# Kernel optimization log

Measured on AMD Instinct MI355X. Metric: run time of the kernel, lower is better.

## Reference

```python
import jax, jax.numpy as jnp
import numpy as np

B, N, K, C = 4, 8192, 16, 128
T = 3  # num_iterations


def _gather(x, idx):
    # x: (B, N, C), idx: (B, N, K) -> (B, N, K, C)
    return jax.vmap(lambda a, i: a[i])(x, idx)


def _linear(x, W, b):
    # torch nn.Linear convention: W is (out, in)
    return x @ W.T + b


def setup_inputs() -> dict:
    key = jax.random.key(0)
    ks = jax.random.split(key, 20)
    s = 0.05
    inp = {
        'xyz': jax.random.normal(ks[0], (B, N, 3), jnp.float32),
        'features': jax.random.normal(ks[1], (B, N, C), jnp.float32),
        'knn_idx': jax.random.randint(ks[2], (B, N, K), 0, N),
        # offset_pred: Linear(C,C) -> ReLU -> Linear(C,3)
        'off_W1': jax.random.normal(ks[3], (C, C), jnp.float32) * s,
        'off_b1': jnp.zeros((C,), jnp.float32),
        'off_W2': jax.random.normal(ks[4], (3, C), jnp.float32) * s,
        'off_b2': jnp.zeros((3,), jnp.float32),
        # per-iteration edge MLP: Linear(3+C, C) -> ReLU -> Linear(C, C)
        'edge_W1': jax.random.normal(ks[5], (T, C, 3 + C), jnp.float32) * s,
        'edge_b1': jnp.zeros((T, C), jnp.float32),
        'edge_W2': jax.random.normal(ks[6], (T, C, C), jnp.float32) * s,
        'edge_b2': jnp.zeros((T, C), jnp.float32),
        # per-iteration update MLP: Linear(2C, C) -> ReLU -> Linear(C, C)
        'upd_W1': jax.random.normal(ks[7], (T, C, 2 * C), jnp.float32) * s,
        'upd_b1': jnp.zeros((T, C), jnp.float32),
        'upd_W2': jax.random.normal(ks[8], (T, C, C), jnp.float32) * s,
        'upd_b2': jnp.zeros((T, C), jnp.float32),
    }
    return inp


def reference(xyz, features, knn_idx, off_W1, off_b1, off_W2, off_b2,
              edge_W1, edge_b1, edge_W2, edge_b2,
              upd_W1, upd_b1, upd_W2, upd_b2):
    n_iter = edge_W1.shape[0]
    for t in range(n_iter):
        delta_xyz = _linear(jax.nn.relu(_linear(features, off_W1, off_b1)), off_W2, off_b2)
        neighbor_xyz = _gather(xyz, knn_idx)          # (B,N,K,3)
        neighbor_feat = _gather(features, knn_idx)    # (B,N,K,C)
        center_xyz = xyz + delta_xyz                  # (B,N,3)
        rel_pos = neighbor_xyz - center_xyz[:, :, None, :]
        edge_input = jnp.concatenate([rel_pos, neighbor_feat], axis=-1)  # (B,N,K,3+C)
        edge_feat = _linear(jax.nn.relu(_linear(edge_input, edge_W1[t], edge_b1[t])), edge_W2[t], edge_b2[t])
        agg_feat = jnp.max(edge_feat, axis=2)         # (B,N,C)
        upd_in = jnp.concatenate([agg_feat, features], axis=-1)
        features = features + _linear(jax.nn.relu(_linear(upd_in, upd_W1[t], upd_b1[t])), upd_W2[t], upd_b2[t])
    return features
```

## Files before the change

kernel.cpp:

```cpp
#include <hip/hip_runtime.h>
#include <cstddef>

#define NB 4
#define NP 8192
#define NK 16
#define NC 128
#define HW_ 136
#define GIW 136
#define AGW 136
#define CW  132
#define UINW 264
#define HUW 136

using short8   = __attribute__((ext_vector_type(8))) short;
using ushort4v = __attribute__((ext_vector_type(4))) unsigned short;
using floatx4  = __attribute__((ext_vector_type(4))) float;

union U8 { short8 s8; unsigned u[4]; };

__device__ __forceinline__ unsigned short f2bf(float f) {
    union { float f; unsigned u; } v; v.f = f;
    unsigned r = v.u + 0x7FFFu + ((v.u >> 16) & 1u);
    return (unsigned short)(r >> 16);
}
__device__ __forceinline__ float bf2f(unsigned short u) {
    union { unsigned u; float f; } v; v.u = ((unsigned)u) << 16;
    return v.f;
}
__device__ __forceinline__ unsigned cvt_pk_bf16(float lo, float hi) {
    unsigned d;
    asm("v_cvt_pk_bf16_f32 %0, %1, %2" : "=v"(d) : "v"(lo), "v"(hi));
    return d;
}

#define MFMA(a, b, c) __builtin_amdgcn_mfma_f32_16x16x32_bf16((a), (b), (c), 0, 0, 0)

__device__ __forceinline__ short8 xform(short8 g, floatx4 ca, floatx4 cb) {
    U8 u;
    u.u[0] = cvt_pk_bf16(fmaxf(bf2f((unsigned short)g[0]) - ca[0], 0.f),
                         fmaxf(bf2f((unsigned short)g[1]) - ca[1], 0.f));
    u.u[1] = cvt_pk_bf16(fmaxf(bf2f((unsigned short)g[2]) - ca[2], 0.f),
                         fmaxf(bf2f((unsigned short)g[3]) - ca[3], 0.f));
    u.u[2] = cvt_pk_bf16(fmaxf(bf2f((unsigned short)g[4]) - cb[0], 0.f),
                         fmaxf(bf2f((unsigned short)g[5]) - cb[1], 0.f));
    u.u[3] = cvt_pk_bf16(fmaxf(bf2f((unsigned short)g[6]) - cb[2], 0.f),
                         fmaxf(bf2f((unsigned short)g[7]) - cb[3], 0.f));
    return u.s8;
}

__global__ void pack_weights_k(const float* __restrict__ offW1,
                               const float* __restrict__ eW1,
                               const float* __restrict__ eW2,
                               const float* __restrict__ uW1,
                               const float* __restrict__ uW2,
                               unsigned short* __restrict__ offW1p,
                               unsigned short* __restrict__ eW1fp,
                               unsigned short* __restrict__ eW2p,
                               unsigned short* __restrict__ uW1p,
                               unsigned short* __restrict__ uW2p)
{
    int i = blockIdx.x * 256 + threadIdx.x;
    if (i < 16384) { offW1p[i] = f2bf(offW1[i]); return; }
    i -= 16384;
    if (i < 49152) {
        int tt = i / 16384, rem = i % 16384;
        int o = rem / 128, k = rem % 128;
        eW1fp[i] = f2bf(eW1[(tt * 128 + o) * 131 + 3 + k]);
        return;
    }
    i -= 49152;
    if (i < 49152) { eW2p[i] = f2bf(eW2[i]); return; }
    i -= 49152;
    if (i < 98304) { uW1p[i] = f2bf(uW1[i]); return; }
    i -= 98304;
    if (i < 49152) { uW2p[i] = f2bf(uW2[i]); }
}

__global__ __launch_bounds__(256, 4)
void center_k(const float* __restrict__ Fin, const float* __restrict__ xyz,
              const unsigned short* __restrict__ offW1p,
              const float* __restrict__ offW2, const float* __restrict__ offb1,
              const float* __restrict__ offb2,
              const unsigned short* __restrict__ eW1fp,
              const float* __restrict__ eW1r0,
              const float* __restrict__ eb1_0,
              unsigned short* __restrict__ Gbf, float* __restrict__ ctr)
{
    __shared__ __align__(16) unsigned short sA[32 * HW_];
    __shared__ __align__(16) unsigned short sH[32 * HW_];
    __shared__ float s_XY[96];
    const int t = threadIdx.x, wv = t >> 6, ln = t & 63, q = ln >> 4, r = ln & 15;
    const int cg0 = wv << 1;
    const int base = blockIdx.x * 32;

    {
        int row = t >> 3, c16 = (t & 7) * 16;
        const float* src = Fin + (size_t)(base + row) * NC + c16;
        float4 f0 = *(const float4*)src;
        float4 f1 = *(const float4*)(src + 4);
        float4 f2 = *(const float4*)(src + 8);
        float4 f3 = *(const float4*)(src + 12);
        short8 u0, u1;
        u0[0]=f2bf(f0.x); u0[1]=f2bf(f0.y); u0[2]=f2bf(f0.z); u0[3]=f2bf(f0.w);
        u0[4]=f2bf(f1.x); u0[5]=f2bf(f1.y); u0[6]=f2bf(f1.z); u0[7]=f2bf(f1.w);
        u1[0]=f2bf(f2.x); u1[1]=f2bf(f2.y); u1[2]=f2bf(f2.z); u1[3]=f2bf(f2.w);
        u1[4]=f2bf(f3.x); u1[5]=f2bf(f3.y); u1[6]=f2bf(f3.z); u1[7]=f2bf(f3.w);
        *(short8*)&sA[row * HW_ + c16]     = u0;
        *(short8*)&sA[row * HW_ + c16 + 8] = u1;
    }
    if (t < 96) s_XY[t] = xyz[(size_t)base * 3 + t];
    __syncthreads();

    floatx4 agk[2][2];
    {
        short8 wo[2][4], wg[2][4];
#pragma unroll
        for (int c = 0; c < 2; ++c)
#pragma unroll
            for (int ks = 0; ks < 4; ++ks) {
                wo[c][ks] = *(const short8*)(offW1p + ((cg0 + c) * 16 + r) * NC + ks * 32 + q * 8);
                wg[c][ks] = *(const short8*)(eW1fp  + ((cg0 + c) * 16 + r) * NC + ks * 32 + q * 8);
            }
        float bo[2] = { offb1[cg0 * 16 + r], offb1[(cg0 + 1) * 16 + r] };
#pragma unroll
        for (int rt = 0; rt < 2; ++rt) {
            short8 af[4];
#pragma unroll
            for (int ks = 0; ks < 4; ++ks)
                af[ks] = *(const short8*)&sA[(rt * 16 + r) * HW_ + ks * 32 + q * 8];
            floatx4 ao[2] = { {0.f,0.f,0.f,0.f}, {0.f,0.f,0.f,0.f} };
            floatx4 ag[2] = { {0.f,0.f,0.f,0.f}, {0.f,0.f,0.f,0.f} };
#pragma unroll
            for (int c = 0; c < 2; ++c)
#pragma unroll
                for (int ks = 0; ks < 4; ++ks) {
                    ao[c] = MFMA(af[ks], wo[c][ks], ao[c]);
                    ag[c] = MFMA(af[ks], wg[c][ks], ag[c]);
                }
#pragma unroll
            for (int c = 0; c < 2; ++c) {
                int col = (cg0 + c) * 16 + r;
#pragma unroll
                for (int i = 0; i < 4; ++i)
                    sH[(rt * 16 + q * 4 + i) * HW_ + col] = f2bf(fmaxf(ao[c][i] + bo[c], 0.f));
                agk[rt][c] = ag[c];
            }
        }
    }
    __syncthreads();

    {
#pragma unroll
        for (int c = 0; c < 2; ++c) {
            int col = (cg0 + c) * 16 + r;
            const float* wN = eW1r0 + (size_t)col * 131;
            float w0 = wN[0], w1 = wN[1], w2 = wN[2], b1v = eb1_0[col];
#pragma unroll
            for (int rt = 0; rt < 2; ++rt)
#pragma unroll
                for (int i = 0; i < 4; ++i) {
                    int row = rt * 16 + q * 4 + i;
                    sA[row * HW_ + col] = f2bf(agk[rt][c][i]
                        + s_XY[row * 3 + 0] * w0 + s_XY[row * 3 + 1] * w1
                        + s_XY[row * 3 + 2] * w2 + b1v);
                }
        }
    }
    if (wv < 2) {
        int rt = wv;
        short8 wf[4];
#pragma unroll
        for (int ks = 0; ks < 4; ++ks) {
            short8 u = {0,0,0,0,0,0,0,0};
            if (r < 3) {
                const float* w = offW2 + r * NC + ks * 32 + q * 8;
                float4 f0 = *(const float4*)w;
                float4 f1 = *(const float4*)(w + 4);
                u[0]=f2bf(f0.x); u[1]=f2bf(f0.y); u[2]=f2bf(f0.z); u[3]=f2bf(f0.w);
                u[4]=f2bf(f1.x); u[5]=f2bf(f1.y); u[6]=f2bf(f1.z); u[7]=f2bf(f1.w);
            }
            wf[ks] = u;
        }
        short8 af[4];
#pragma unroll
        for (int ks = 0; ks < 4; ++ks)
            af[ks] = *(const short8*)&sH[(rt * 16 + r) * HW_ + ks * 32 + q * 8];
        floatx4 acc = {0.f, 0.f, 0.f, 0.f};
#pragma unroll
        for (int ks = 0; ks < 4; ++ks)
            acc = MFMA(af[ks], wf[ks], acc);
        if (r < 3) {
#pragma unroll
            for (int i = 0; i < 4; ++i) {
                int p = rt * 16 + q * 4 + i;
                ctr[(size_t)(base + p) * 3 + r] =
                    xyz[(size_t)(base + p) * 3 + r] + acc[i] + offb2[r];
            }
        }
    }
    __syncthreads();

    {
        int row = t >> 3, c16 = (t & 7) * 16;
        *(short8*)(Gbf + (size_t)(base + row) * NC + c16)     = *(short8*)&sA[row * HW_ + c16];
        *(short8*)(Gbf + (size_t)(base + row) * NC + c16 + 8) = *(short8*)&sA[row * HW_ + c16 + 8];
    }
}

__global__ __launch_bounds__(256, 2)
void edge_k(const unsigned short* __restrict__ Gbf,
            const int* __restrict__ knn,
            const float* __restrict__ ctr,
            const float* __restrict__ eW1rC,
            const float* __restrict__ eb2,
            const unsigned short* __restrict__ eW2p,
            unsigned short* __restrict__ aggG)
{
    __shared__ __align__(16) unsigned short s_H[64 * GIW];
    __shared__ __align__(16) float s_C[8 * CW];
    __shared__ __align__(16) unsigned short s_AGB[8 * AGW];

    const int xcd  = blockIdx.x & 7;
    const int slot = blockIdx.x >> 3;
    const int b    = xcd >> 1;
    const int n0   = ((slot << 1) | (xcd & 1)) << 3;
    const int t = threadIdx.x, wv = t >> 6, ln = t & 63;
    const int q = ln >> 4, r = ln & 15, cg0 = wv << 1;
    const int base = b * NP + n0;
    const int rr = t >> 4, c8 = (t & 15) * 8;

    const int* kb = knn + (size_t)base * NK;
    int kn[8];
#pragma unroll
    for (int j = 0; j < 8; ++j) kn[j] = kb[j * 16 + rr];
    short8 g0[4];
#pragma unroll
    for (int p = 0; p < 4; ++p)
        g0[p] = *(const short8*)(Gbf + (size_t)(b * NP + kn[p]) * NC + c8);

    short8 wf2[2][4];
#pragma unroll
    for (int c = 0; c < 2; ++c)
#pragma unroll
        for (int ks = 0; ks < 4; ++ks)
            wf2[c][ks] = *(const short8*)(eW2p + ((cg0 + c) * 16 + r) * NC + ks * 32 + q * 8);
    float eb2v[2] = { eb2[cg0 * 16 + r], eb2[(cg0 + 1) * 16 + r] };

    {
        int p = t >> 5, c0 = (t & 31) * 4;
        float cx = ctr[(size_t)(base + p) * 3 + 0];
        float cy = ctr[(size_t)(base + p) * 3 + 1];
        float cz = ctr[(size_t)(base + p) * 3 + 2];
#pragma unroll
        for (int k = 0; k < 4; ++k) {
            int col = c0 + k;
            const float* w = eW1rC + (size_t)col * 131;
            s_C[p * CW + col] = cx * w[0] + cy * w[1] + cz * w[2];
        }
    }
    __syncthreads();

#pragma unroll
    for (int p = 0; p < 4; ++p) {
        const float* cp = &s_C[p * CW + c8];
        floatx4 ca = *(const floatx4*)(cp);
        floatx4 cb = *(const floatx4*)(cp + 4);
        *(short8*)&s_H[(p * 16 + rr) * GIW + c8] = xform(g0[p], ca, cb);
    }
    short8 g1[4];
#pragma unroll
    for (int p = 0; p < 4; ++p)
        g1[p] = *(const short8*)(Gbf + (size_t)(b * NP + kn[4 + p]) * NC + c8);
    __syncthreads();

#pragma unroll
    for (int rt = 0; rt < 4; ++rt) {
        short8 af[4];
#pragma unroll
        for (int ks = 0; ks < 4; ++ks)
            af[ks] = *(const short8*)&s_H[(rt * 16 + r) * GIW + ks * 32 + q * 8];
        floatx4 acc[2] = { {0.f,0.f,0.f,0.f}, {0.f,0.f,0.f,0.f} };
#pragma unroll
        for (int c = 0; c < 2; ++c)
#pragma unroll
            for (int ks = 0; ks < 4; ++ks)
                acc[c] = MFMA(af[ks], wf2[c][ks], acc[c]);
#pragma unroll
        for (int c = 0; c < 2; ++c) {
            float m = fmaxf(fmaxf(acc[c][0], acc[c][1]), fmaxf(acc[c][2], acc[c][3]));
            m = fmaxf(m, __shfl_xor(m, 16));
            m = fmaxf(m, __shfl_xor(m, 32));
            if (q == 0)
                s_AGB[rt * AGW + (cg0 + c) * 16 + r] = f2bf(m + eb2v[c]);
        }
    }
    __syncthreads();

#pragma unroll
    for (int p = 0; p < 4; ++p) {
        const float* cp = &s_C[(4 + p) * CW + c8];
        floatx4 ca = *(const floatx4*)(cp);
        floatx4 cb = *(const floatx4*)(cp + 4);
        *(short8*)&s_H[(p * 16 + rr) * GIW + c8] = xform(g1[p], ca, cb);
    }
    __syncthreads();

#pragma unroll
    for (int rt = 0; rt < 4; ++rt) {
        short8 af[4];
#pragma unroll
        for (int ks = 0; ks < 4; ++ks)
            af[ks] = *(const short8*)&s_H[(rt * 16 + r) * GIW + ks * 32 + q * 8];
        floatx4 acc[2] = { {0.f,0.f,0.f,0.f}, {0.f,0.f,0.f,0.f} };
#pragma unroll
        for (int c = 0; c < 2; ++c)
#pragma unroll
            for (int ks = 0; ks < 4; ++ks)
                acc[c] = MFMA(af[ks], wf2[c][ks], acc[c]);
#pragma unroll
        for (int c = 0; c < 2; ++c) {
            float m = fmaxf(fmaxf(acc[c][0], acc[c][1]), fmaxf(acc[c][2], acc[c][3]));
            m = fmaxf(m, __shfl_xor(m, 16));
            m = fmaxf(m, __shfl_xor(m, 32));
            if (q == 0)
                s_AGB[(4 + rt) * AGW + (cg0 + c) * 16 + r] = f2bf(m + eb2v[c]);
        }
    }
    __syncthreads();

    if (t < 128) {
        int row = t >> 4, cc = (t & 15) * 8;
        *(short8*)(aggG + (size_t)(base + row) * NC + cc) = *(short8*)&s_AGB[row * AGW + cc];
    }
}

__global__ __launch_bounds__(256, 3)
void upd_k(const float* __restrict__ Fin, float* __restrict__ Fout,
           const unsigned short* __restrict__ aggG,
           const float* __restrict__ xyz,
           const unsigned short* __restrict__ uW1p,
           const unsigned short* __restrict__ uW2p,
           const float* __restrict__ ub1, const float* __restrict__ ub2,
           const unsigned short* __restrict__ eW1fpN,
           const float* __restrict__ eW1rN,
           const float* __restrict__ eb1N,
           const unsigned short* __restrict__ offW1p,
           const float* __restrict__ offW2, const float* __restrict__ offb1,
           const float* __restrict__ offb2,
           unsigned short* __restrict__ Gbf, float* __restrict__ ctrOut,
           int doNext)
{
    __shared__ __align__(16) unsigned short s_UIN[32 * UINW];
    __shared__ __align__(16) unsigned short s_H[32 * HUW];
    __shared__ __align__(16) unsigned short s_FN[32 * HUW];
    __shared__ float s_XY[96];

    const int xcd  = blockIdx.x & 7;
    const int slot = blockIdx.x >> 3;
    const int b    = xcd >> 1;
    const int n0   = ((slot << 1) | (xcd & 1)) << 5;
    const int t = threadIdx.x, wv = t >> 6, ln = t & 63;
    const int q = ln >> 4, r = ln & 15, cg0 = wv << 1;
    const int base = b * NP + n0;
    const int row32 = t >> 3, c16 = (t & 7) * 16;

    {
        const unsigned short* ap = aggG + (size_t)(base + row32) * NC + c16;
        *(short8*)&s_UIN[row32 * UINW + c16]     = *(const short8*)ap;
        *(short8*)&s_UIN[row32 * UINW + c16 + 8] = *(const short8*)(ap + 8);
        const float* src = Fin + (size_t)(base + row32) * NC + c16;
        float4 f0 = *(const float4*)src;
        float4 f1 = *(const float4*)(src + 4);
        float4 f2 = *(const float4*)(src + 8);
        float4 f3 = *(const float4*)(src + 12);
        short8 u0, u1;
        u0[0]=f2bf(f0.x); u0[1]=f2bf(f0.y); u0[2]=f2bf(f0.z); u0[3]=f2bf(f0.w);
        u0[4]=f2bf(f1.x); u0[5]=f2bf(f1.y); u0[6]=f2bf(f1.z); u0[7]=f2bf(f1.w);
        u1[0]=f2bf(f2.x); u1[1]=f2bf(f2.y); u1[2]=f2bf(f2.z); u1[3]=f2bf(f2.w);
        u1[4]=f2bf(f3.x); u1[5]=f2bf(f3.y); u1[6]=f2bf(f3.z); u1[7]=f2bf(f3.w);
        *(short8*)&s_UIN[row32 * UINW + 128 + c16]     = u0;
        *(short8*)&s_UIN[row32 * UINW + 128 + c16 + 8] = u1;
    }
    if (t < 96) s_XY[t] = xyz[(size_t)base * 3 + t];
    __syncthreads();

    {
        short8 wfa[2][8];
#pragma unroll
        for (int c = 0; c < 2; ++c)
#pragma unroll
            for (int ks = 0; ks < 8; ++ks)
                wfa[c][ks] = *(const short8*)(uW1p + ((cg0 + c) * 16 + r) * 256 + ks * 32 + q * 8);
        float ub1v[2] = { ub1[cg0 * 16 + r], ub1[(cg0 + 1) * 16 + r] };
#pragma unroll
        for (int rt = 0; rt < 2; ++rt) {
            short8 af[8];
#pragma unroll
            for (int ks = 0; ks < 8; ++ks)
                af[ks] = *(const short8*)&s_UIN[(rt * 16 + r) * UINW + ks * 32 + q * 8];
            floatx4 acc3[2] = { {0.f,0.f,0.f,0.f}, {0.f,0.f,0.f,0.f} };
#pragma unroll
            for (int c = 0; c < 2; ++c)
#pragma unroll
                for (int ks = 0; ks < 8; ++ks)
                    acc3[c] = MFMA(af[ks], wfa[c][ks], acc3[c]);
#pragma unroll
            for (int c = 0; c < 2; ++c)
#pragma unroll
                for (int i = 0; i < 4; ++i)
                    s_H[(rt * 16 + q * 4 + i) * HUW + (cg0 + c) * 16 + r] =
                        f2bf(fmaxf(acc3[c][i] + ub1v[c], 0.f));
        }
    }
    __syncthreads();

    {
        short8 wfb[2][4];
#pragma unroll
        for (int c = 0; c < 2; ++c)
#pragma unroll
            for (int ks = 0; ks < 4; ++ks)
                wfb[c][ks] = *(const short8*)(uW2p + ((cg0 + c) * 16 + r) * NC + ks * 32 + q * 8);
        float ub2v[2] = { ub2[cg0 * 16 + r], ub2[(cg0 + 1) * 16 + r] };
#pragma unroll
        for (int rt = 0; rt < 2; ++rt) {
            short8 af[4];
#pragma unroll
            for (int ks = 0; ks < 4; ++ks)
                af[ks] = *(const short8*)&s_H[(rt * 16 + r) * HUW + ks * 32 + q * 8];
            floatx4 acc[2] = { {0.f,0.f,0.f,0.f}, {0.f,0.f,0.f,0.f} };
#pragma unroll
            for (int c = 0; c < 2; ++c)
#pragma unroll
                for (int ks = 0; ks < 4; ++ks)
                    acc[c] = MFMA(af[ks], wfb[c][ks], acc[c]);
#pragma unroll
            for (int c = 0; c < 2; ++c) {
                int col = (cg0 + c) * 16 + r;
#pragma unroll
                for (int i = 0; i < 4; ++i) {
                    int p = rt * 16 + q * 4 + i;
                    float fnew = Fin[(size_t)(base + p) * NC + col] + acc[c][i] + ub2v[c];
                    Fout[(size_t)(base + p) * NC + col] = fnew;
                    s_FN[p * HUW + col] = f2bf(fnew);
                }
            }
        }
    }

    if (doNext) {
        __syncthreads();
        {
            short8 wg[2][4], wo[2][4];
#pragma unroll
            for (int c = 0; c < 2; ++c)
#pragma unroll
                for (int ks = 0; ks < 4; ++ks) {
                    wg[c][ks] = *(const short8*)(eW1fpN + ((cg0 + c) * 16 + r) * NC + ks * 32 + q * 8);
                    wo[c][ks] = *(const short8*)(offW1p + ((cg0 + c) * 16 + r) * NC + ks * 32 + q * 8);
                }
            float bo[2] = { offb1[cg0 * 16 + r], offb1[(cg0 + 1) * 16 + r] };
#pragma unroll
            for (int rt = 0; rt < 2; ++rt) {
                short8 af[4];
#pragma unroll
                for (int ks = 0; ks < 4; ++ks)
                    af[ks] = *(const short8*)&s_FN[(rt * 16 + r) * HUW + ks * 32 + q * 8];
                floatx4 ag[2] = { {0.f,0.f,0.f,0.f}, {0.f,0.f,0.f,0.f} };
                floatx4 ao[2] = { {0.f,0.f,0.f,0.f}, {0.f,0.f,0.f,0.f} };
#pragma unroll
                for (int c = 0; c < 2; ++c)
#pragma unroll
                    for (int ks = 0; ks < 4; ++ks) {
                        ag[c] = MFMA(af[ks], wg[c][ks], ag[c]);
                        ao[c] = MFMA(af[ks], wo[c][ks], ao[c]);
                    }
#pragma unroll
                for (int c = 0; c < 2; ++c) {
                    int col = (cg0 + c) * 16 + r;
                    const float* wN = eW1rN + (size_t)col * 131;
                    float w0 = wN[0], w1 = wN[1], w2 = wN[2], b1v = eb1N[col];
#pragma unroll
                    for (int i = 0; i < 4; ++i) {
                        int p = rt * 16 + q * 4 + i;
                        s_UIN[p * UINW + col] = f2bf(ag[c][i]
                            + s_XY[p * 3 + 0] * w0 + s_XY[p * 3 + 1] * w1
                            + s_XY[p * 3 + 2] * w2 + b1v);
                        s_H[p * HUW + col]    = f2bf(fmaxf(ao[c][i] + bo[c], 0.f));
                    }
                }
            }
        }
        __syncthreads();

        *(short8*)(Gbf + (size_t)(base + row32) * NC + c16) =
            *(short8*)&s_UIN[row32 * UINW + c16];
        *(short8*)(Gbf + (size_t)(base + row32) * NC + c16 + 8) =
            *(short8*)&s_UIN[row32 * UINW + c16 + 8];

        if (wv < 2) {
            int rt = wv;
            short8 wf[4];
#pragma unroll
            for (int ks = 0; ks < 4; ++ks) {
                short8 u = {0,0,0,0,0,0,0,0};
                if (r < 3) {
                    const float* w = offW2 + r * NC + ks * 32 + q * 8;
                    float4 f0 = *(const float4*)w;
                    float4 f1 = *(const float4*)(w + 4);
                    u[0]=f2bf(f0.x); u[1]=f2bf(f0.y); u[2]=f2bf(f0.z); u[3]=f2bf(f0.w);
                    u[4]=f2bf(f1.x); u[5]=f2bf(f1.y); u[6]=f2bf(f1.z); u[7]=f2bf(f1.w);
                }
                wf[ks] = u;
            }
            short8 af[4];
#pragma unroll
            for (int ks = 0; ks < 4; ++ks)
                af[ks] = *(const short8*)&s_H[(rt * 16 + r) * HUW + ks * 32 + q * 8];
            floatx4 acc = {0.f, 0.f, 0.f, 0.f};
#pragma unroll
            for (int ks = 0; ks < 4; ++ks)
                acc = MFMA(af[ks], wf[ks], acc);
            if (r < 3) {
#pragma unroll
                for (int i = 0; i < 4; ++i) {
                    int p = rt * 16 + q * 4 + i;
                    ctrOut[(size_t)(base + p) * 3 + r] =
                        xyz[(size_t)(base + p) * 3 + r] + acc[i] + offb2[r];
                }
            }
        }
    }
}

extern "C" void kernel_launch(void* const* d_in, const int* in_sizes, int n_in,
                              void* d_out, int out_size, void* d_ws, size_t ws_size,
                              hipStream_t stream)
{
    const float* xyz   = (const float*)d_in[0];
    const float* feat  = (const float*)d_in[1];
    const int*   knn   = (const int*)d_in[2];
    const float* offW1 = (const float*)d_in[3];
    const float* offb1 = (const float*)d_in[4];
    const float* offW2 = (const float*)d_in[5];
    const float* offb2 = (const float*)d_in[6];
    const float* eW1   = (const float*)d_in[7];
    const float* eb1   = (const float*)d_in[8];
    const float* eW2   = (const float*)d_in[9];
    const float* eb2   = (const float*)d_in[10];
    const float* uW1   = (const float*)d_in[11];
    const float* ub1   = (const float*)d_in[12];
    const float* uW2   = (const float*)d_in[13];
    const float* ub2   = (const float*)d_in[14];
    float* out = (float*)d_out;

    char* ws = (char*)d_ws;
    unsigned short* Gbf    = (unsigned short*)ws;
    float*          ctrb   = (float*)(ws + 8388608);
    unsigned short* offW1p = (unsigned short*)(ws + 8781824);
    unsigned short* eW1fp  = (unsigned short*)(ws + 8814592);
    unsigned short* eW2p   = (unsigned short*)(ws + 8912896);
    unsigned short* uW1p   = (unsigned short*)(ws + 9011200);
    unsigned short* uW2p   = (unsigned short*)(ws + 9207808);
    unsigned short* aggG   = (unsigned short*)(ws + 9306112);

    pack_weights_k<<<1024, 256, 0, stream>>>(offW1, eW1, eW2, uW1, uW2,
                                             offW1p, eW1fp, eW2p, uW1p, uW2p);

    center_k<<<1024, 256, 0, stream>>>(feat, xyz, offW1p, offW2,
                                       offb1, offb2, eW1fp, eW1, eb1,
                                       Gbf, ctrb);

    for (int tt = 0; tt < 3; ++tt) {
        int ntt = (tt + 1) % 3;
        edge_k<<<4096, 256, 0, stream>>>(
            Gbf, knn, ctrb,
            eW1 + (size_t)tt * 128 * 131, eb2 + tt * 128,
            eW2p + tt * 16384, aggG);
        const float* fin = (tt == 0) ? feat : out;
        upd_k<<<1024, 256, 0, stream>>>(
            fin, out, aggG, xyz,
            uW1p + tt * 32768, uW2p + tt * 16384, ub1 + tt * 128, ub2 + tt * 128,
            eW1fp + ntt * 16384, eW1 + (size_t)ntt * 128 * 131, eb1 + ntt * 128,
            offW1p, offW2, offb1, offb2,
            Gbf, ctrb, (tt < 2) ? 1 : 0);
    }
}
```

Before: 295.9 us.

## Restructure edge kernel to gather neighbors directly into MFMA A-fragments per wave

The edge kernel now handles 16 points per block with half as many blocks. Each wave owns four points, gathers neighbor features straight into MFMA A-operand registers, and loops over all 8 output column groups using the W2 weights staged once in shared memory. This removes the s_H shared-memory staging and several block barriers, and amortizes the W2 load over more points. In exchange it uses more LDS per block (the full 128x136 W2 tile) and issues per-lane 16-byte gathers that may coalesce less well.

```diff
diff --git a/kernel.cpp b/kernel.cpp
--- a/kernel.cpp
+++ b/kernel.cpp
@@ -6,7 +6,7 @@
 #define NK 16
 #define NC 128
 #define HW_ 136
-#define GIW 136
+#define SW2 136
 #define AGW 136
 #define CW  132
 #define UINW 264
@@ -216,119 +216,86 @@
             const unsigned short* __restrict__ eW2p,
             unsigned short* __restrict__ aggG)
 {
-    __shared__ __align__(16) unsigned short s_H[64 * GIW];
-    __shared__ __align__(16) float s_C[8 * CW];
-    __shared__ __align__(16) unsigned short s_AGB[8 * AGW];
+    __shared__ __align__(16) unsigned short s_W2[128 * SW2];
+    __shared__ __align__(16) float s_C[16 * CW];
+    __shared__ __align__(16) unsigned short s_AGB[16 * AGW];
 
     const int xcd  = blockIdx.x & 7;
     const int slot = blockIdx.x >> 3;
     const int b    = xcd >> 1;
-    const int n0   = ((slot << 1) | (xcd & 1)) << 3;
+    const int n0   = ((slot << 1) | (xcd & 1)) << 4;
     const int t = threadIdx.x, wv = t >> 6, ln = t & 63;
-    const int q = ln >> 4, r = ln & 15, cg0 = wv << 1;
+    const int q = ln >> 4, r = ln & 15;
     const int base = b * NP + n0;
-    const int rr = t >> 4, c8 = (t & 15) * 8;
-
-    const int* kb = knn + (size_t)base * NK;
-    int kn[8];
-#pragma unroll
-    for (int j = 0; j < 8; ++j) kn[j] = kb[j * 16 + rr];
-    short8 g0[4];
-#pragma unroll
-    for (int p = 0; p < 4; ++p)
-        g0[p] = *(const short8*)(Gbf + (size_t)(b * NP + kn[p]) * NC + c8);
-
-    short8 wf2[2][4];
-#pragma unroll
-    for (int c = 0; c < 2; ++c)
-#pragma unroll
-        for (int ks = 0; ks < 4; ++ks)
-            wf2[c][ks] = *(const short8*)(eW2p + ((cg0 + c) * 16 + r) * NC + ks * 32 + q * 8);
-    float eb2v[2] = { eb2[cg0 * 16 + r], eb2[(cg0 + 1) * 16 + r] };
-
-    {
-        int p = t >> 5, c0 = (t & 31) * 4;
+    const int wp0 = wv << 2;
+
+    {
+        int row = t >> 1, c64 = (t & 1) << 6;
+        const unsigned short* src = eW2p + row * NC + c64;
+#pragma unroll
+        for (int g = 0; g < 8; ++g)
+            *(short8*)&s_W2[row * SW2 + c64 + g * 8] = *(const short8*)(src + g * 8);
+    }
+    {
+        int p = t >> 4, c0 = (t & 15) * 8;
         float cx = ctr[(size_t)(base + p) * 3 + 0];
         float cy = ctr[(size_t)(base + p) * 3 + 1];
         float cz = ctr[(size_t)(base + p) * 3 + 2];
 #pragma unroll
-        for (int k = 0; k < 4; ++k) {
+        for (int k = 0; k < 8; ++k) {
             int col = c0 + k;
             const float* w = eW1rC + (size_t)col * 131;
             s_C[p * CW + col] = cx * w[0] + cy * w[1] + cz * w[2];
         }
     }
-    __syncthreads();
-
-#pragma unroll
-    for (int p = 0; p < 4; ++p) {
-        const float* cp = &s_C[p * CW + c8];
-        floatx4 ca = *(const floatx4*)(cp);
-        floatx4 cb = *(const floatx4*)(cp + 4);
-        *(short8*)&s_H[(p * 16 + rr) * GIW + c8] = xform(g0[p], ca, cb);
-    }
-    short8 g1[4];
+    float ebv[8];
+#pragma unroll
+    for (int c = 0; c < 8; ++c) ebv[c] = eb2[c * 16 + r];
+    int kn[4];
 #pragma unroll
     for (int p = 0; p < 4; ++p)
-        g1[p] = *(const short8*)(Gbf + (size_t)(b * NP + kn[4 + p]) * NC + c8);
-    __syncthreads();
-
-#pragma unroll
-    for (int rt = 0; rt < 4; ++rt) {
-        short8 af[4];
-#pragma unroll
-        for (int ks = 0; ks < 4; ++ks)
-            af[ks] = *(const short8*)&s_H[(rt * 16 + r) * GIW + ks * 32 + q * 8];
-        floatx4 acc[2] = { {0.f,0.f,0.f,0.f}, {0.f,0.f,0.f,0.f} };
-#pragma unroll
-        for (int c = 0; c < 2; ++c)
+        kn[p] = knn[(size_t)(base + wp0 + p) * NK + r];
+    __syncthreads();
+
+#pragma unroll
+    for (int pair = 0; pair < 2; ++pair) {
+        short8 haf[2][4];
+#pragma unroll
+        for (int pp = 0; pp < 2; ++pp) {
+            int p = pair * 2 + pp;
+            const unsigned short* gp = Gbf + (size_t)(b * NP + kn[p]) * NC + q * 8;
+            const float* cp = &s_C[(wp0 + p) * CW + q * 8];
+#pragma unroll
+            for (int ks = 0; ks < 4; ++ks) {
+                short8 g = *(const short8*)(gp + ks * 32);
+                floatx4 ca = *(const floatx4*)(cp + ks * 32);
+                floatx4 cb = *(const floatx4*)(cp + ks * 32 + 4);
+                haf[pp][ks] = xform(g, ca, cb);
+            }
+        }
+#pragma unroll
+        for (int c = 0; c < 8; ++c) {
+            short8 bf[4];
 #pragma unroll
             for (int ks = 0; ks < 4; ++ks)
-                acc[c] = MFMA(af[ks], wf2[c][ks], acc[c]);
-#pragma unroll
-        for (int c = 0; c < 2; ++c) {
-            float m = fmaxf(fmaxf(acc[c][0], acc[c][1]), fmaxf(acc[c][2], acc[c][3]));
-            m = fmaxf(m, __shfl_xor(m, 16));
-            m = fmaxf(m, __shfl_xor(m, 32));
-            if (q == 0)
-                s_AGB[rt * AGW + (cg0 + c) * 16 + r] = f2bf(m + eb2v[c]);
-        }
-    }
-    __syncthreads();
-
-#pragma unroll
-    for (int p = 0; p < 4; ++p) {
-        const float* cp = &s_C[(4 + p) * CW + c8];
-        floatx4 ca = *(const floatx4*)(cp);
-        floatx4 cb = *(const floatx4*)(cp + 4);
-        *(short8*)&s_H[(p * 16 + rr) * GIW + c8] = xform(g1[p], ca, cb);
-    }
-    __syncthreads();
-
-#pragma unroll
-    for (int rt = 0; rt < 4; ++rt) {
-        short8 af[4];
-#pragma unroll
-        for (int ks = 0; ks < 4; ++ks)
-            af[ks] = *(const short8*)&s_H[(rt * 16 + r) * GIW + ks * 32 + q * 8];
-        floatx4 acc[2] = { {0.f,0.f,0.f,0.f}, {0.f,0.f,0.f,0.f} };
-#pragma unroll
-        for (int c = 0; c < 2; ++c)
-#pragma unroll
-            for (int ks = 0; ks < 4; ++ks)
-                acc[c] = MFMA(af[ks], wf2[c][ks], acc[c]);
-#pragma unroll
-        for (int c = 0; c < 2; ++c) {
-            float m = fmaxf(fmaxf(acc[c][0], acc[c][1]), fmaxf(acc[c][2], acc[c][3]));
-            m = fmaxf(m, __shfl_xor(m, 16));
-            m = fmaxf(m, __shfl_xor(m, 32));
-            if (q == 0)
-                s_AGB[(4 + rt) * AGW + (cg0 + c) * 16 + r] = f2bf(m + eb2v[c]);
-        }
-    }
-    __syncthreads();
-
-    if (t < 128) {
+                bf[ks] = *(const short8*)&s_W2[(c * 16 + r) * SW2 + ks * 32 + q * 8];
+#pragma unroll
+            for (int pp = 0; pp < 2; ++pp) {
+                floatx4 acc = {0.f, 0.f, 0.f, 0.f};
+#pragma unroll
+                for (int ks = 0; ks < 4; ++ks)
+                    acc = MFMA(haf[pp][ks], bf[ks], acc);
+                float m = fmaxf(fmaxf(acc[0], acc[1]), fmaxf(acc[2], acc[3]));
+                m = fmaxf(m, __shfl_xor(m, 16));
+                m = fmaxf(m, __shfl_xor(m, 32));
+                if (q == 0)
+                    s_AGB[(wp0 + pair * 2 + pp) * AGW + c * 16 + r] = f2bf(m + ebv[c]);
+            }
+        }
+    }
+    __syncthreads();
+
+    {
         int row = t >> 4, cc = (t & 15) * 8;
         *(short8*)(aggG + (size_t)(base + row) * NC + cc) = *(short8*)&s_AGB[row * AGW + cc];
     }
@@ -573,7 +540,7 @@
 
     for (int tt = 0; tt < 3; ++tt) {
         int ntt = (tt + 1) % 3;
-        edge_k<<<4096, 256, 0, stream>>>(
+        edge_k<<<2048, 256, 0, stream>>>(
             Gbf, knn, ctrb,
             eW1 + (size_t)tt * 128 * 131, eb2 + tt * 128,
             eW2p + tt * 16384, aggG);
```

After: 321.7 us. 8.7% more time.
